# Kernel optimization log

Measured on AMD Instinct MI355X. Metric: run time of the kernel, lower is better.

Reference implementation:

```python
import jax, jax.numpy as jnp
import numpy as np

D_MODEL = 1024
NUM_HEADS = 16
THETA = 10000.0
BATCH = 2
SEQ = 2048


def setup_inputs() -> dict:
    key = jax.random.key(0)
    ks = jax.random.split(key, 5)
    std = (2.0 / (D_MODEL + D_MODEL)) ** 0.5
    mk = lambda k: jax.random.truncated_normal(k, -3.0, 3.0, (D_MODEL, D_MODEL), jnp.float32) * std
    return {
        'x': jax.random.normal(ks[0], (BATCH, SEQ, D_MODEL), jnp.float32),
        'Wq': mk(ks[1]),
        'Wk': mk(ks[2]),
        'Wv': mk(ks[3]),
        'Wo': mk(ks[4]),
        'token_positions': jnp.arange(SEQ, dtype=jnp.int32),
    }


def _apply_rope(x, token_positions, theta):
    # x: (B, H, S, d_k)
    d_k = x.shape[-1]
    freq = 1.0 / theta ** (jnp.arange(0, d_k, 2, dtype=jnp.float32) / d_k)  # (d_k//2,)
    freqs = token_positions.astype(jnp.float32)[:, None] * freq[None, :]   # (S, d_k//2)
    cos, sin = jnp.cos(freqs), jnp.sin(freqs)
    x_real = x[..., 0::2]
    x_imag = x[..., 1::2]
    rot_real = x_real * cos - x_imag * sin
    rot_imag = x_real * sin + x_imag * cos
    # interleave back: (..., d_k//2, 2) -> (..., d_k)
    out = jnp.stack([rot_real, rot_imag], axis=-1)
    return out.reshape(x.shape)


def reference(x, Wq, Wk, Wv, Wo, token_positions):
    B, S, D = x.shape
    H = NUM_HEADS
    d_k = D // H

    def split_heads(t):
        return t.reshape(B, S, H, d_k).transpose(0, 2, 1, 3)  # (B, H, S, d_k)

    Q = split_heads(jnp.einsum('bsd,od->bso', x, Wq))
    K = split_heads(jnp.einsum('bsd,od->bso', x, Wk))
    V = split_heads(jnp.einsum('bsd,od->bso', x, Wv))

    Q = _apply_rope(Q, token_positions, THETA)
    K = _apply_rope(K, token_positions, THETA)

    # naive materialized attention with causal mask, faithful to source
    scores = jnp.einsum('bhqd,bhkd->bhqk', Q, K)
    causal = jnp.tril(jnp.ones((S, S), dtype=bool))  # True = attend
    scores = jnp.where(causal[None, None], scores, -jnp.inf)
    scores = scores / jnp.sqrt(jnp.asarray(d_k, scores.dtype))
    probs = jax.nn.softmax(scores, axis=-1)
    attn = jnp.einsum('bhqk,bhkd->bhqd', probs, V)  # (B, H, S, d_v)

    attn = attn.transpose(0, 2, 1, 3).reshape(B, S, D)
    return jnp.einsum('bsd,od->bso', attn, Wo)
```

## Files before the change

kernel.cpp:

```cpp
#include <hip/hip_runtime.h>
#include <hip/hip_bf16.h>
#include <math.h>

#define NUM_HEADS 16
#define DK 64
#define SEQ 2048
#define BATCHN 2
#define DM 1024
#define BS (BATCHN*SEQ)
#define LSCALE 0.18033688011112042f

typedef __bf16 bf16x8 __attribute__((ext_vector_type(8)));
typedef float floatx4 __attribute__((ext_vector_type(4)));
typedef unsigned short ushort;
typedef unsigned int uint;

__device__ __forceinline__ ushort f2bu(float f){
    union { __hip_bfloat16 h; ushort u; } cv; cv.h = __float2bfloat16(f); return cv.u;
}
__device__ __forceinline__ uint packbf(float a, float b){
    return (uint)f2bu(a) | ((uint)f2bu(b) << 16);
}
__device__ __forceinline__ float bu2f(ushort u){
    union { uint u; float f; } cv; cv.u = (uint)u << 16; return cv.f;
}
__device__ __forceinline__ uint cvtpk(float lo, float hi){
    uint r; asm("v_cvt_pk_bf16_f32 %0, %1, %2" : "=v"(r) : "v"(lo), "v"(hi));
    return r;
}
__device__ __forceinline__ void gl16(const void* g, void* l){
    __builtin_amdgcn_global_load_lds(
        (const __attribute__((address_space(1))) unsigned int*)g,
        (__attribute__((address_space(3))) unsigned int*)l, 16, 0, 0);
}

__global__ __launch_bounds__(256)
void castall(const float* __restrict__ x,  const float* __restrict__ wq,
             const float* __restrict__ wk, const float* __restrict__ wv,
             const float* __restrict__ wo, const int* __restrict__ pos,
             ushort* __restrict__ xb, ushort* __restrict__ wqkb,
             ushort* __restrict__ wvb, ushort* __restrict__ wob,
             float2* __restrict__ tab)
{
    int bid = blockIdx.x;
    if (bid >= 4096) {
        int idx = (bid - 4096)*256 + threadIdx.x;
        int s = idx >> 5, i = idx & 31;
        float invf = expf(-0.28782313662425575f * (float)i);
        float ang = (float)pos[s] * invf;
        float sn, cs; sincosf(ang, &sn, &cs);
        tab[idx] = make_float2(cs, sn);
        return;
    }
    const float* src; ushort* dst; int off;
    if (bid < 2048)      { src = x;  dst = xb;             off = bid; }
    else if (bid < 2560) { src = wq; dst = wqkb;           off = bid - 2048; }
    else if (bid < 3072) { src = wk; dst = wqkb + 1048576; off = bid - 2560; }
    else if (bid < 3584) { src = wv; dst = wvb;            off = bid - 3072; }
    else                 { src = wo; dst = wob;            off = bid - 3584; }
    int i = off*2048 + threadIdx.x*8;
    float4 a = *(const float4*)(src+i);
    float4 b = *(const float4*)(src+i+4);
    uint4 o;
    o.x = packbf(a.x, a.y);
    o.y = packbf(a.z, a.w);
    o.z = packbf(b.x, b.y);
    o.w = packbf(b.z, b.w);
    *(uint4*)(dst+i) = o;
}

__global__ __launch_bounds__(256)
void proj_fused(const ushort* __restrict__ xb, const ushort* __restrict__ Wqkb,
                const ushort* __restrict__ Wvb, ushort* __restrict__ Qb,
                ushort* __restrict__ VTp, const float2* __restrict__ rope)
{
    __shared__ ushort As[128][32];
    __shared__ ushort Bs[128][32];

    const int bx = blockIdx.x;
    int bid;
    if (bx < 512) {
        const int xcd = bx & 7, i = bx >> 3;
        const int tr = (xcd >> 1)*8 + (i >> 3);
        const int tc = (xcd & 1)*8 + (i & 7);
        bid = tr*16 + tc;
    } else {
        const int j = bx - 512;
        const int xcd = j & 7, i = j >> 3;
        const int tr = i >> 2;
        const int tc = xcd*4 + (i & 3);
        bid = 512 + tr*32 + tc;
    }

    const ushort* A; const ushort* W; int row0, col0, mode;
    if (bid < 512) { A = xb;  W = Wqkb; row0 = (bid >> 4) * 128;
                     col0 = (bid & 15) * 128;  mode = 1; }
    else           { int i = bid - 512; A = Wvb; W = xb;
                     row0 = (i >> 5) * 128; col0 = (i & 31) * 128; mode = 2; }

    const int t = threadIdx.x;
    const int w = t >> 6;
    const int L = t & 63;
    const int lr = L & 15;
    const int lq = L >> 4;
    const int wrow = w * 32;

    floatx4 acc[2][8];
    #pragma unroll
    for (int i = 0; i < 2; ++i)
        #pragma unroll
        for (int j = 0; j < 8; ++j)
            acc[i][j] = (floatx4){0.f,0.f,0.f,0.f};

    const int rr = t >> 2, ko = (t & 3) * 8;
    const ushort* ga = A + (size_t)(row0 + rr) * DM + ko;
    const ushort* gb = W + (size_t)(col0 + rr) * DM + ko;

    for (int k0 = 0; k0 < DM; k0 += 32) {
        __syncthreads();
        gl16(ga + k0,                    &As[rr][ko]);
        gl16(ga + k0 + (size_t)64*DM,    &As[rr + 64][ko]);
        gl16(gb + k0,                    &Bs[rr][ko]);
        gl16(gb + k0 + (size_t)64*DM,    &Bs[rr + 64][ko]);
        __syncthreads();

        bf16x8 aF0 = *(const bf16x8*)&As[wrow + lr][lq*8];
        bf16x8 aF1 = *(const bf16x8*)&As[wrow + 16 + lr][lq*8];
        #pragma unroll
        for (int tc = 0; tc < 8; ++tc) {
            bf16x8 bF = *(const bf16x8*)&Bs[tc*16 + lr][lq*8];
            acc[0][tc] = __builtin_amdgcn_mfma_f32_16x16x32_bf16(aF0, bF, acc[0][tc], 0, 0, 0);
            acc[1][tc] = __builtin_amdgcn_mfma_f32_16x16x32_bf16(aF1, bF, acc[1][tc], 0, 0, 0);
        }
    }

    if (mode == 2) {
        #pragma unroll
        for (int tr = 0; tr < 2; ++tr)
            #pragma unroll
            for (int tc = 0; tc < 8; ++tc)
                #pragma unroll
                for (int r = 0; r < 4; ++r) {
                    int m = row0 + wrow + tr*16 + lq*4 + r;
                    int c = col0 + tc*16 + lr;
                    VTp[(size_t)m * BS + c] = f2bu(acc[tr][tc][r]);
                }
    } else {
        const int mat = col0 >> 10;
        const int base_hh = (col0 & 1023) >> 6;
        ushort* out = Qb + (size_t)mat * (BATCHN*NUM_HEADS*SEQ*DK);
        const float qscale = mat ? 1.f : LSCALE;
        #pragma unroll
        for (int tr = 0; tr < 2; ++tr)
            #pragma unroll
            for (int tc = 0; tc < 8; ++tc)
                #pragma unroll
                for (int r = 0; r < 4; ++r) {
                    int m = row0 + wrow + tr*16 + lq*4 + r;
                    int b = m >> 11;
                    int s = m & (SEQ - 1);
                    int dd = (tc*16 + lr) & 63;
                    int hh = base_hh + (tc >> 2);
                    float v = acc[tr][tc][r];
                    float o = __shfl_xor(v, 1, 64);
                    float2 cs = rope[s*32 + (dd >> 1)];
                    float rv = (dd & 1) ? fmaf(o, cs.y,  v * cs.x)
                                        : fmaf(-o, cs.y, v * cs.x);
                    out[((size_t)((b*NUM_HEADS + hh)*SEQ + s))*DK + dd] =
                        f2bu(rv * qscale);
                }
    }
}

__global__ __launch_bounds__(256)
void gemm_out(const ushort* __restrict__ A, const ushort* __restrict__ W,
              float* __restrict__ out)
{
    __shared__ ushort As[128][32];
    __shared__ ushort Bs[64][32];

    const int t = threadIdx.x;
    const int w = t >> 6;
    const int L = t & 63;
    const int lr = L & 15;
    const int lq = L >> 4;
    const int row0 = blockIdx.y * 128;
    const int col0 = blockIdx.x * 64;
    const int wrow = w * 32;

    floatx4 acc[2][4];
    #pragma unroll
    for (int i = 0; i < 2; ++i)
        #pragma unroll
        for (int j = 0; j < 4; ++j)
            acc[i][j] = (floatx4){0.f,0.f,0.f,0.f};

    const int rr = t >> 2, ko = (t & 3) * 8;
    const ushort* ga = A + (size_t)(row0 + rr) * DM + ko;
    const ushort* gb = W + (size_t)(col0 + rr) * DM + ko;

    for (int k0 = 0; k0 < DM; k0 += 32) {
        __syncthreads();
        gl16(ga + k0,                 &As[rr][ko]);
        gl16(ga + k0 + (size_t)64*DM, &As[rr + 64][ko]);
        gl16(gb + k0,                 &Bs[rr][ko]);
        __syncthreads();

        bf16x8 aF0 = *(const bf16x8*)&As[wrow + lr][lq*8];
        bf16x8 aF1 = *(const bf16x8*)&As[wrow + 16 + lr][lq*8];
        #pragma unroll
        for (int tc = 0; tc < 4; ++tc) {
            bf16x8 bF = *(const bf16x8*)&Bs[tc*16 + lr][lq*8];
            acc[0][tc] = __builtin_amdgcn_mfma_f32_16x16x32_bf16(aF0, bF, acc[0][tc], 0, 0, 0);
            acc[1][tc] = __builtin_amdgcn_mfma_f32_16x16x32_bf16(aF1, bF, acc[1][tc], 0, 0, 0);
        }
    }

    #pragma unroll
    for (int tr = 0; tr < 2; ++tr)
        #pragma unroll
        for (int tc = 0; tc < 4; ++tc)
            #pragma unroll
            for (int r = 0; r < 4; ++r) {
                int m = row0 + wrow + tr*16 + lq*4 + r;
                int c = col0 + tc*16 + lr;
                out[(size_t)m * DM + c] = acc[tr][tc][r];
            }
}

__global__ __launch_bounds__(128)
void attn_mfma(const ushort* __restrict__ Qb, const ushort* __restrict__ Kb,
               const ushort* __restrict__ VT, ushort* __restrict__ attnb,
               ushort* __restrict__ Opart, float* __restrict__ lpart)
{
    __shared__ ushort Ks[64*64];
    __shared__ ushort Vs[64*64];

    const int t = threadIdx.x;
    const int w = t >> 6;
    const int L = t & 63;
    const int lr = L & 15, lq = L >> 4;
    const int h  = blockIdx.y;
    const int b  = blockIdx.z;

    int qt, chunk, nch;
    {
        const int bx = blockIdx.x;
        if (bx < 8)       { qt = bx;              chunk = 0;     nch = 1; }
        else if (bx < 24) { int i = bx - 8;  qt = 8  + (i>>1); chunk = i&1;        nch = 2; }
        else if (bx < 48) { int i = bx - 24; int q3 = i/3; qt = 16 + q3; chunk = i - q3*3; nch = 3; }
        else              { int i = bx - 48; qt = 24 + (i>>2); chunk = i&3;        nch = 4; }
    }
    const int nt = qt + 1;
    const int t0 = (nt * chunk) / nch;
    const int t1 = (nt * (chunk + 1)) / nch;
    const int q0 = qt * 64;
    const int qw = q0 + w * 32;
    const size_t qkbase = (size_t)(b*NUM_HEADS + h) * SEQ * DK;

    bf16x8 qA0, qA1, qB0, qB1;
    {
        const ushort* qp = Qb + qkbase + (size_t)(qw + lr) * DK + lq*8;
        qA0 = *(const bf16x8*)qp;
        qA1 = *(const bf16x8*)(qp + 32);
        qB0 = *(const bf16x8*)(qp + 16*DK);
        qB1 = *(const bf16x8*)(qp + 16*DK + 32);
    }

    bf16x8 ones8;
    {
        union { uint u[4]; bf16x8 v; } o;
        o.u[0] = o.u[1] = o.u[2] = o.u[3] = 0x3f803f80u;
        ones8 = o.v;
    }

    floatx4 O0[4], O1[4];
    #pragma unroll
    for (int g = 0; g < 4; ++g) {
        O0[g] = (floatx4){0.f,0.f,0.f,0.f};
        O1[g] = (floatx4){0.f,0.f,0.f,0.f};
    }
    floatx4 lA = (floatx4){0.f,0.f,0.f,0.f};
    floatx4 lB = (floatx4){0.f,0.f,0.f,0.f};

    const int sr = t >> 3, t7 = t & 7;
    const int kwb  = (sr*64 + t7*8) ^ ((sr & 7) << 3);
    const int pc0  = ((t7 >> 2) << 3) | ((t7 & 1) << 2) | ((t7 >> 1) & 1);
    const int vwb0 = (sr*64 + pc0*4)     ^ ((sr & 7) << 3);
    const int vwb1 = (sr*64 + pc0*4 + 8) ^ ((sr & 7) << 3);
    const ushort* kpt = Kb + qkbase + (size_t)sr * DK + t7*8;
    const ushort* vpt = VT + ((size_t)(h*DK + sr)) * BS + b*SEQ + t7*8;

    const int kro0 = (lr*64 + lq*8)      ^ ((lr & 7) << 3);
    const int kro1 = (lr*64 + 32 + lq*8) ^ ((lr & 7) << 3);

    uint4 kv0, kv1, kv2, kv3, vv0, vv1, vv2, vv3;

#define GLOAD(T)                                                              \
    {                                                                         \
        const ushort* kg = kpt + (size_t)(T) * 64 * DK;                       \
        const ushort* vg = vpt + (T) * 64;                                    \
        kv0 = *(const uint4*)(kg);                                            \
        kv1 = *(const uint4*)(kg + 16*DK);                                    \
        kv2 = *(const uint4*)(kg + 32*DK);                                    \
        kv3 = *(const uint4*)(kg + 48*DK);                                    \
        vv0 = *(const uint4*)(vg);                                            \
        vv1 = *(const uint4*)(vg + (size_t)16*BS);                            \
        vv2 = *(const uint4*)(vg + (size_t)32*BS);                            \
        vv3 = *(const uint4*)(vg + (size_t)48*BS);                            \
    }

#define STAGE()                                                               \
    {                                                                         \
        *(uint4*)&Ks[kwb]        = kv0;                                       \
        *(uint4*)&Ks[kwb + 1024] = kv1;                                       \
        *(uint4*)&Ks[kwb + 2048] = kv2;                                       \
        *(uint4*)&Ks[kwb + 3072] = kv3;                                       \
        *(uint2*)&Vs[vwb0]        = make_uint2(vv0.x, vv0.y);                 \
        *(uint2*)&Vs[vwb1]        = make_uint2(vv0.z, vv0.w);                 \
        *(uint2*)&Vs[vwb0 + 1024] = make_uint2(vv1.x, vv1.y);                 \
        *(uint2*)&Vs[vwb1 + 1024] = make_uint2(vv1.z, vv1.w);                 \
        *(uint2*)&Vs[vwb0 + 2048] = make_uint2(vv2.x, vv2.y);                 \
        *(uint2*)&Vs[vwb1 + 2048] = make_uint2(vv2.z, vv2.w);                 \
        *(uint2*)&Vs[vwb0 + 3072] = make_uint2(vv3.x, vv3.y);                 \
        *(uint2*)&Vs[vwb1 + 3072] = make_uint2(vv3.z, vv3.w);                 \
    }

#define COMPUTE(LASTT)                                                        \
    {                                                                         \
        uint2 pk0[4], pk1[4];                                                 \
        _Pragma("unroll")                                                     \
        for (int g = 0; g < 4; ++g) {                                         \
            bf16x8 kf0 = *(const bf16x8*)&Ks[kro0 + g*1024];                  \
            bf16x8 kf1 = *(const bf16x8*)&Ks[kro1 + g*1024];                  \
            floatx4 s0 = (floatx4){0.f,0.f,0.f,0.f};                          \
            s0 = __builtin_amdgcn_mfma_f32_16x16x32_bf16(kf0, qA0, s0,0,0,0); \
            s0 = __builtin_amdgcn_mfma_f32_16x16x32_bf16(kf1, qA1, s0,0,0,0); \
            floatx4 s1 = (floatx4){0.f,0.f,0.f,0.f};                          \
            s1 = __builtin_amdgcn_mfma_f32_16x16x32_bf16(kf0, qB0, s1,0,0,0); \
            s1 = __builtin_amdgcn_mfma_f32_16x16x32_bf16(kf1, qB1, s1,0,0,0); \
            float a0 = __builtin_amdgcn_exp2f(s0[0]);                         \
            float a1 = __builtin_amdgcn_exp2f(s0[1]);                         \
            float a2 = __builtin_amdgcn_exp2f(s0[2]);                         \
            float a3 = __builtin_amdgcn_exp2f(s0[3]);                         \
            float b0 = __builtin_amdgcn_exp2f(s1[0]);                         \
            float b1 = __builtin_amdgcn_exp2f(s1[1]);                         \
            float b2 = __builtin_amdgcn_exp2f(s1[2]);                         \
            float b3 = __builtin_amdgcn_exp2f(s1[3]);                         \
            if (LASTT) {                                                      \
                const int kbase = g*16 + lq*4;                                \
                a0 = (kbase + 0 <= lim0) ? a0 : 0.f;                          \
                a1 = (kbase + 1 <= lim0) ? a1 : 0.f;                          \
                a2 = (kbase + 2 <= lim0) ? a2 : 0.f;                          \
                a3 = (kbase + 3 <= lim0) ? a3 : 0.f;                          \
                b0 = (kbase + 0 <= lim1) ? b0 : 0.f;                          \
                b1 = (kbase + 1 <= lim1) ? b1 : 0.f;                          \
                b2 = (kbase + 2 <= lim1) ? b2 : 0.f;                          \
                b3 = (kbase + 3 <= lim1) ? b3 : 0.f;                          \
            }                                                                 \
            pk0[g] = make_uint2(cvtpk(a0, a1), cvtpk(a2, a3));                \
            pk1[g] = make_uint2(cvtpk(b0, b1), cvtpk(b2, b3));                \
        }                                                                     \
        _Pragma("unroll")                                                     \
        for (int c = 0; c < 2; ++c) {                                         \
            union { uint u[4]; bf16x8 v; } a0u, a1u;                          \
            a0u.u[0] = pk0[2*c].x;   a0u.u[1] = pk0[2*c].y;                   \
            a0u.u[2] = pk0[2*c+1].x; a0u.u[3] = pk0[2*c+1].y;                 \
            a1u.u[0] = pk1[2*c].x;   a1u.u[1] = pk1[2*c].y;                   \
            a1u.u[2] = pk1[2*c+1].x; a1u.u[3] = pk1[2*c+1].y;                 \
            lA = __builtin_amdgcn_mfma_f32_16x16x32_bf16(a0u.v, ones8, lA,0,0,0); \
            lB = __builtin_amdgcn_mfma_f32_16x16x32_bf16(a1u.v, ones8, lB,0,0,0); \
            const int vro = c ? kro1 : kro0;                                  \
            _Pragma("unroll")                                                 \
            for (int g2 = 0; g2 < 4; ++g2) {                                  \
                bf16x8 vf = *(const bf16x8*)&Vs[vro + g2*1024];               \
                O0[g2] = __builtin_amdgcn_mfma_f32_16x16x32_bf16(a0u.v, vf, O0[g2],0,0,0); \
                O1[g2] = __builtin_amdgcn_mfma_f32_16x16x32_bf16(a1u.v, vf, O1[g2],0,0,0); \
            }                                                                 \
        }                                                                     \
    }

    GLOAD(t0);
    const bool haslast = (t1 == nt);
    const int tmain = haslast ? t1 - 1 : t1;
    {
        const int lim0 = 0, lim1 = 0;
        for (int tile = t0; tile < tmain; ++tile) {
            __syncthreads();
            STAGE();
            __syncthreads();
            if (tile + 1 < t1) GLOAD(tile + 1);
            COMPUTE(false);
        }
    }
    if (haslast) {
        __syncthreads();
        STAGE();
        __syncthreads();
        const int lim0 = qw + lr - (nt - 1)*64;
        const int lim1 = lim0 + 16;
        COMPUTE(true);
    }
#undef GLOAD
#undef STAGE
#undef COMPUTE

    if (nch == 1) {
        #pragma unroll
        for (int r = 0; r < 4; ++r) {
            float li0 = 1.f / lA[r];
            float li1 = 1.f / lB[r];
            int s0r = qw + lq*4 + r;
            int s1r = qw + 16 + lq*4 + r;
            #pragma unroll
            for (int g2 = 0; g2 < 4; ++g2) {
                attnb[((size_t)(b*SEQ + s0r))*DM + h*DK + g2*16 + lr] = f2bu(O0[g2][r] * li0);
                attnb[((size_t)(b*SEQ + s1r))*DM + h*DK + g2*16 + lr] = f2bu(O1[g2][r] * li1);
            }
        }
    } else {
        const int slot = ((b*NUM_HEADS + h)*24 + (qt - 8))*4 + chunk;
        ushort* Op = Opart + (size_t)slot * 4096;
        #pragma unroll
        for (int r = 0; r < 4; ++r) {
            int ql0 = w*32 + lq*4 + r;
            int ql1 = w*32 + 16 + lq*4 + r;
            #pragma unroll
            for (int g2 = 0; g2 < 4; ++g2) {
                Op[ql0*64 + g2*16 + lr] = f2bu(O0[g2][r]);
                Op[ql1*64 + g2*16 + lr] = f2bu(O1[g2][r]);
            }
        }
        if (lr == 0) {
            #pragma unroll
            for (int r = 0; r < 4; ++r) {
                lpart[(size_t)slot*64 + w*32 + lq*4 + r]      = lA[r];
                lpart[(size_t)slot*64 + w*32 + 16 + lq*4 + r] = lB[r];
            }
        }
    }
}

__global__ __launch_bounds__(256)
void combine(const ushort* __restrict__ Opart, const float* __restrict__ lpart,
             ushort* __restrict__ attnb)
{
    int gx = blockIdx.x;
    int qti = gx % 24, bh = gx / 24;
    int h = bh & 15, b = bh >> 4;
    int qt = 8 + qti;
    int nch = (qt >> 3) + 1;
    int tid = threadIdx.x;
    int row = tid >> 2, c0 = (tid & 3) * 16;
    const int base_slot = (bh*24 + qti)*4;

    float acc[16];
    #pragma unroll
    for (int e = 0; e < 16; ++e) acc[e] = 0.f;
    float l = 0.f;

    for (int c = 0; c < nch; ++c) {
        const ushort* Op = Opart + (size_t)(base_slot + c)*4096 + row*64 + c0;
        uint4 u0 = *(const uint4*)(Op);
        uint4 u1 = *(const uint4*)(Op + 8);
        const ushort* h0 = (const ushort*)&u0;
        const ushort* h1 = (const ushort*)&u1;
        #pragma unroll
        for (int e = 0; e < 8; ++e) { acc[e]   += bu2f(h0[e]); }
        #pragma unroll
        for (int e = 0; e < 8; ++e) { acc[8+e] += bu2f(h1[e]); }
        l += lpart[(size_t)(base_slot + c)*64 + row];
    }
    float li = 1.f / l;
    int s = qt*64 + row;
    ushort* dst = attnb + ((size_t)(b*SEQ + s))*DM + h*DK + c0;
    #pragma unroll
    for (int e = 0; e < 16; ++e) dst[e] = f2bu(acc[e] * li);
}

extern "C" void kernel_launch(void* const* d_in, const int* in_sizes, int n_in,
                              void* d_out, int out_size, void* d_ws, size_t ws_size,
                              hipStream_t stream) {
    const float* x   = (const float*)d_in[0];
    const float* Wq  = (const float*)d_in[1];
    const float* Wk  = (const float*)d_in[2];
    const float* Wv  = (const float*)d_in[3];
    const float* Wo  = (const float*)d_in[4];
    const int*   pos = (const int*)d_in[5];
    float* out = (float*)d_out;

    const size_t MB = 1u << 20;
    char* ws = (char*)d_ws;
    ushort* xb    = (ushort*)(ws);
    ushort* Wqkb  = (ushort*)(ws +  8*MB);
    ushort* Wvb   = (ushort*)(ws + 12*MB);
    ushort* Opart = (ushort*)(ws);
    float*  lpart = (float*)(ws + 24*MB);
    ushort* Qb    = (ushort*)(ws + 25*MB);
    ushort* Kb    = (ushort*)(ws + 33*MB);
    ushort* VT    = (ushort*)(ws + 41*MB);
    ushort* attnb = (ushort*)(ws + 49*MB);
    float2* ropeT = (float2*)(ws + 57*MB);
    ushort* Wob   = (ushort*)(ws + 58*MB);

    dim3 blk(256);
    castall<<<4352, blk, 0, stream>>>(x, Wq, Wk, Wv, Wo, pos,
                                      xb, Wqkb, Wvb, Wob, ropeT);

    proj_fused<<<768, blk, 0, stream>>>(xb, Wqkb, Wvb, Qb, VT, ropeT);

    attn_mfma<<<dim3(80, NUM_HEADS, BATCHN), dim3(128), 0, stream>>>(Qb, Kb, VT, attnb,
                                                                     Opart, lpart);
    combine<<<768, blk, 0, stream>>>(Opart, lpart, attnb);

    gemm_out<<<dim3(16,32), blk, 0, stream>>>(attnb, Wob, out);
}
```

Before: 192.6 us.

## Widen GEMM K-tile to 64 with XOR-swizzled shared memory layout

Both the fused QKV projection and the output projection GEMMs now stage a 64-wide K slice per iteration instead of 32, halving the number of barrier pairs per tile. Shared memory is laid out as 64-element rows with an XOR swizzle on 16-byte chunks, applied at the global-load side, to avoid LDS bank conflicts on the fragment reads. This doubles LDS usage per block, which may lower occupancy.

```diff
diff --git a/kernel.cpp b/kernel.cpp
--- a/kernel.cpp
+++ b/kernel.cpp
@@ -74,8 +74,8 @@
                 const ushort* __restrict__ Wvb, ushort* __restrict__ Qb,
                 ushort* __restrict__ VTp, const float2* __restrict__ rope)
 {
-    __shared__ ushort As[128][32];
-    __shared__ ushort Bs[128][32];
+    __shared__ ushort As[128*64];
+    __shared__ ushort Bs[128*64];
 
     const int bx = blockIdx.x;
     int bid;
@@ -112,25 +112,36 @@
         for (int j = 0; j < 8; ++j)
             acc[i][j] = (floatx4){0.f,0.f,0.f,0.f};
 
-    const int rr = t >> 2, ko = (t & 3) * 8;
+    const int rr = t >> 3;
+    const int ko = ((t & 7) ^ (rr & 7)) * 8;
     const ushort* ga = A + (size_t)(row0 + rr) * DM + ko;
     const ushort* gb = W + (size_t)(col0 + rr) * DM + ko;
-
-    for (int k0 = 0; k0 < DM; k0 += 32) {
+    ushort* Asl = As + t*8;
+    ushort* Bsl = Bs + t*8;
+
+    for (int k0 = 0; k0 < DM; k0 += 64) {
         __syncthreads();
-        gl16(ga + k0,                    &As[rr][ko]);
-        gl16(ga + k0 + (size_t)64*DM,    &As[rr + 64][ko]);
-        gl16(gb + k0,                    &Bs[rr][ko]);
-        gl16(gb + k0 + (size_t)64*DM,    &Bs[rr + 64][ko]);
+        gl16(ga + k0,                 Asl);
+        gl16(ga + k0 + (size_t)32*DM, Asl + 2048);
+        gl16(ga + k0 + (size_t)64*DM, Asl + 4096);
+        gl16(ga + k0 + (size_t)96*DM, Asl + 6144);
+        gl16(gb + k0,                 Bsl);
+        gl16(gb + k0 + (size_t)32*DM, Bsl + 2048);
+        gl16(gb + k0 + (size_t)64*DM, Bsl + 4096);
+        gl16(gb + k0 + (size_t)96*DM, Bsl + 6144);
         __syncthreads();
 
-        bf16x8 aF0 = *(const bf16x8*)&As[wrow + lr][lq*8];
-        bf16x8 aF1 = *(const bf16x8*)&As[wrow + 16 + lr][lq*8];
-        #pragma unroll
-        for (int tc = 0; tc < 8; ++tc) {
-            bf16x8 bF = *(const bf16x8*)&Bs[tc*16 + lr][lq*8];
-            acc[0][tc] = __builtin_amdgcn_mfma_f32_16x16x32_bf16(aF0, bF, acc[0][tc], 0, 0, 0);
-            acc[1][tc] = __builtin_amdgcn_mfma_f32_16x16x32_bf16(aF1, bF, acc[1][tc], 0, 0, 0);
+        #pragma unroll
+        for (int h = 0; h < 2; ++h) {
+            const int co = (lq*8 + h*32) ^ ((lr & 7) << 3);
+            bf16x8 aF0 = *(const bf16x8*)&As[(wrow + lr)*64 + co];
+            bf16x8 aF1 = *(const bf16x8*)&As[(wrow + 16 + lr)*64 + co];
+            #pragma unroll
+            for (int tc = 0; tc < 8; ++tc) {
+                bf16x8 bF = *(const bf16x8*)&Bs[(tc*16 + lr)*64 + co];
+                acc[0][tc] = __builtin_amdgcn_mfma_f32_16x16x32_bf16(aF0, bF, acc[0][tc], 0, 0, 0);
+                acc[1][tc] = __builtin_amdgcn_mfma_f32_16x16x32_bf16(aF1, bF, acc[1][tc], 0, 0, 0);
+            }
         }
     }
 
@@ -176,8 +187,8 @@
 void gemm_out(const ushort* __restrict__ A, const ushort* __restrict__ W,
               float* __restrict__ out)
 {
-    __shared__ ushort As[128][32];
-    __shared__ ushort Bs[64][32];
+    __shared__ ushort As[128*64];
+    __shared__ ushort Bs[64*64];
 
     const int t = threadIdx.x;
     const int w = t >> 6;
@@ -195,24 +206,34 @@
         for (int j = 0; j < 4; ++j)
             acc[i][j] = (floatx4){0.f,0.f,0.f,0.f};
 
-    const int rr = t >> 2, ko = (t & 3) * 8;
+    const int rr = t >> 3;
+    const int ko = ((t & 7) ^ (rr & 7)) * 8;
     const ushort* ga = A + (size_t)(row0 + rr) * DM + ko;
     const ushort* gb = W + (size_t)(col0 + rr) * DM + ko;
-
-    for (int k0 = 0; k0 < DM; k0 += 32) {
+    ushort* Asl = As + t*8;
+    ushort* Bsl = Bs + t*8;
+
+    for (int k0 = 0; k0 < DM; k0 += 64) {
         __syncthreads();
-        gl16(ga + k0,                 &As[rr][ko]);
-        gl16(ga + k0 + (size_t)64*DM, &As[rr + 64][ko]);
-        gl16(gb + k0,                 &Bs[rr][ko]);
+        gl16(ga + k0,                 Asl);
+        gl16(ga + k0 + (size_t)32*DM, Asl + 2048);
+        gl16(ga + k0 + (size_t)64*DM, Asl + 4096);
+        gl16(ga + k0 + (size_t)96*DM, Asl + 6144);
+        gl16(gb + k0,                 Bsl);
+        gl16(gb + k0 + (size_t)32*DM, Bsl + 2048);
         __syncthreads();
 
-        bf16x8 aF0 = *(const bf16x8*)&As[wrow + lr][lq*8];
-        bf16x8 aF1 = *(const bf16x8*)&As[wrow + 16 + lr][lq*8];
-        #pragma unroll
-        for (int tc = 0; tc < 4; ++tc) {
-            bf16x8 bF = *(const bf16x8*)&Bs[tc*16 + lr][lq*8];
-            acc[0][tc] = __builtin_amdgcn_mfma_f32_16x16x32_bf16(aF0, bF, acc[0][tc], 0, 0, 0);
-            acc[1][tc] = __builtin_amdgcn_mfma_f32_16x16x32_bf16(aF1, bF, acc[1][tc], 0, 0, 0);
+        #pragma unroll
+        for (int h = 0; h < 2; ++h) {
+            const int co = (lq*8 + h*32) ^ ((lr & 7) << 3);
+            bf16x8 aF0 = *(const bf16x8*)&As[(wrow + lr)*64 + co];
+            bf16x8 aF1 = *(const bf16x8*)&As[(wrow + 16 + lr)*64 + co];
+            #pragma unroll
+            for (int tc = 0; tc < 4; ++tc) {
+                bf16x8 bF = *(const bf16x8*)&Bs[(tc*16 + lr)*64 + co];
+                acc[0][tc] = __builtin_amdgcn_mfma_f32_16x16x32_bf16(aF0, bF, acc[0][tc], 0, 0, 0);
+                acc[1][tc] = __builtin_amdgcn_mfma_f32_16x16x32_bf16(aF1, bF, acc[1][tc], 0, 0, 0);
+            }
         }
     }
 
```

Result: no change. 189.4 us (-1.6%).
